# Kernel optimization log

Hardware: AMD Instinct MI355X
Metric: run time of the kernel (lower is better)

Reference implementation:

```python
import jax, jax.numpy as jnp
import numpy as np

# Module hyperparameters (init_kwargs)
NCE_K = 256      # samples per example (col 0 = positive)
NCE_T = 0.07     # temperature
EPS = 1e-7

# Problem sizes
B = 4096         # batch
D = 128          # embedding dim
N = 1_000_000    # memory bank size


def setup_inputs() -> dict:
    key = jax.random.key(0)
    k1, k2, k3, k4 = jax.random.split(key, 4)
    x = jax.random.normal(k1, (B, D), dtype=jnp.float32)
    targets = jax.random.randint(k2, (B,), 0, N)
    memory = jax.random.normal(k3, (N, D), dtype=jnp.float32) * 0.05
    # uniform multinomial-with-replacement sampling == uniform randint
    indices = jax.random.randint(k4, (B, NCE_K), 0, N)
    return {"x": x, "targets": targets, "memory": memory, "indices": indices}


def reference(x, targets, memory, indices):
    # nce_average: overwrite column 0 with the positive index
    idx = indices.at[:, 0].set(targets)              # [B, K]
    weight = memory[idx]                              # [B, K, D] gather
    logits = jnp.einsum('bkd,bd->bk', weight, x) / NCE_T
    sims = jnp.exp(logits)                            # [B, K]
    sims = sims / jnp.sum(sims, axis=1, keepdims=True) * (NCE_K / N)

    # NCE loss: K' = nce_k - 1 noise samples per example
    Kp = NCE_K - 1
    noise = Kp / N
    lnPmt = sims[:, 0] / (sims[:, 0] + noise + EPS)   # [B]
    lnPon = noise / (sims[:, 1:] + noise + EPS)       # [B, K-1]
    loss = -(jnp.log(lnPmt).mean() + jnp.log(lnPon).sum(axis=1).mean())
    return loss
```

## Files before the change

kernel.cpp:

```cpp
#include <hip/hip_runtime.h>

#define B_SZ   4096
#define D_SZ   128
#define K_SZ   256
#define NBUCK  4096
#define BCAP   1024

constexpr float INV_T    = 1.0f / 0.07f;
constexpr float NOISE    = 255.0f / 1000000.0f;
constexpr float EPS_C    = 1e-7f;
constexpr float K_OVER_N = 256.0f / 1000000.0f;


__global__ __launch_bounds__(256) void zero_counters(int* __restrict__ cnt)
{
    const int i = blockIdx.x * 256 + threadIdx.x;
    if (i < NBUCK) cnt[i] = 0;
}

__global__ __launch_bounds__(256, 8) void bin_samples(
    const int* __restrict__ targets,
    const int* __restrict__ indices,
    int*                 __restrict__ cnt,
    unsigned long long*  __restrict__ ent)
{
    const int i = blockIdx.x * 256 + threadIdx.x;
    const int b = i >> 8;
    const int k = i & (K_SZ - 1);
    const int row = (k == 0) ? targets[b] : indices[i];
    const int bu  = row >> 8;
    const int slot = atomicAdd(&cnt[bu], 1);
    if (slot < BCAP)
        ent[(size_t)bu * BCAP + slot] =
            ((unsigned long long)(unsigned)row << 32) | (unsigned)i;
}

__global__ __launch_bounds__(256, 4) void gather_dot(
    const float* __restrict__ x,
    const float* __restrict__ memory,
    const int*                __restrict__ cnt,
    const unsigned long long* __restrict__ ent,
    float*       __restrict__ esims)
{
    const int bu = blockIdx.x;
    const int nb = min(cnt[bu], BCAP);
    if (nb == 0) return;

    const int tid = threadIdx.x;
    const int g   = tid >> 3;
    const int s   = tid & 7;

    for (int base = 0; base < nb; base += 32) {
        const int e  = base + g;
        const int ec = min(e, nb - 1);
        const unsigned long long pk = ent[(size_t)bu * BCAP + ec];
        const int i   = (int)(pk & 0xffffffffu);
        const int row = (int)(pk >> 32);

        const float4* __restrict__ rp =
            (const float4*)(memory + (size_t)row * D_SZ);
        const float4* __restrict__ xp =
            (const float4*)(x + (size_t)(i >> 8) * D_SZ);

        const float4 r0 = rp[0 * 8 + s];
        const float4 r1 = rp[1 * 8 + s];
        const float4 r2 = rp[2 * 8 + s];
        const float4 r3 = rp[3 * 8 + s];
        const float4 x0 = xp[0 * 8 + s];
        const float4 x1 = xp[1 * 8 + s];
        const float4 x2 = xp[2 * 8 + s];
        const float4 x3 = xp[3 * 8 + s];

        float a0 = 0.f, a1 = 0.f;
        a0 = fmaf(r0.x, x0.x, fmaf(r0.y, x0.y, fmaf(r0.z, x0.z, fmaf(r0.w, x0.w, a0))));
        a1 = fmaf(r1.x, x1.x, fmaf(r1.y, x1.y, fmaf(r1.z, x1.z, fmaf(r1.w, x1.w, a1))));
        a0 = fmaf(r2.x, x2.x, fmaf(r2.y, x2.y, fmaf(r2.z, x2.z, fmaf(r2.w, x2.w, a0))));
        a1 = fmaf(r3.x, x3.x, fmaf(r3.y, x3.y, fmaf(r3.z, x3.z, fmaf(r3.w, x3.w, a1))));
        float p = a0 + a1;

        p += __shfl_xor(p, 1, 64);
        p += __shfl_xor(p, 2, 64);
        p += __shfl_xor(p, 4, 64);

        if (s == 0 && e < nb)
            esims[i] = expf(p * INV_T);
    }
}

__global__ __launch_bounds__(256, 8) void reduce_loss(
    const float* __restrict__ esims,
    float*       __restrict__ partial)
{
    __shared__ float s_red[4];
    const int b    = blockIdx.x;
    const int tid  = threadIdx.x;
    const int lane = tid & 63;
    const int wave = tid >> 6;

    const float e = esims[(size_t)b * K_SZ + tid];

    float sum = e;
    #pragma unroll
    for (int m = 32; m >= 1; m >>= 1)
        sum += __shfl_xor(sum, m, 64);
    if (lane == 0) s_red[wave] = sum;
    __syncthreads();
    const float S = s_red[0] + s_red[1] + s_red[2] + s_red[3];

    const float sims = e * (K_OVER_N / S);
    float term = (tid == 0)
        ? logf(sims / (sims + NOISE + EPS_C))
        : logf(NOISE / (sims + NOISE + EPS_C));

    #pragma unroll
    for (int m = 32; m >= 1; m >>= 1)
        term += __shfl_xor(term, m, 64);
    __syncthreads();
    if (lane == 0) s_red[wave] = term;
    __syncthreads();
    if (tid == 0)
        partial[b] = s_red[0] + s_red[1] + s_red[2] + s_red[3];
}

__global__ __launch_bounds__(256) void nce_final(
    const float* __restrict__ partial, float* __restrict__ out)
{
    const int tid = threadIdx.x;
    float s = 0.0f;
    #pragma unroll
    for (int i = tid; i < B_SZ; i += 256)
        s += partial[i];
    #pragma unroll
    for (int m = 32; m >= 1; m >>= 1)
        s += __shfl_xor(s, m, 64);
    __shared__ float sr[4];
    if ((tid & 63) == 0) sr[tid >> 6] = s;
    __syncthreads();
    if (tid == 0)
        out[0] = -(sr[0] + sr[1] + sr[2] + sr[3]) / (float)B_SZ;
}

extern "C" void kernel_launch(void* const* d_in, const int* in_sizes, int n_in,
                              void* d_out, int out_size, void* d_ws, size_t ws_size,
                              hipStream_t stream) {
    const float* x       = (const float*)d_in[0];
    const int*   targets = (const int*)  d_in[1];
    const float* memory  = (const float*)d_in[2];
    const int*   indices = (const int*)  d_in[3];
    float* out = (float*)d_out;

    char* ws = (char*)d_ws;
    int*                cnt     = (int*)ws;
    unsigned long long* ent     = (unsigned long long*)(ws + 16384);
    float*              esims   = (float*)(ws + 16384 + (size_t)NBUCK * BCAP * 8);
    float*              partial = esims + (size_t)B_SZ * K_SZ;

    zero_counters<<<NBUCK / 256, 256, 0, stream>>>(cnt);
    bin_samples<<<(B_SZ * K_SZ) / 256, 256, 0, stream>>>(targets, indices, cnt, ent);
    gather_dot<<<NBUCK, 256, 0, stream>>>(x, memory, cnt, ent, esims);
    reduce_loss<<<B_SZ, 256, 0, stream>>>(esims, partial);
    nce_final<<<1, 256, 0, stream>>>(partial, out);
}
```

Measured before the change: 743.2 us.

## Stage contiguous 64-row memory tiles in LDS instead of random row gathers

Buckets shrink to 64 consecutive memory rows, and each gather_dot block first streams its whole tile into padded shared memory, then computes the dot products from LDS. This turns scattered row gathers into coalesced streaming reads of the full table. It adds about 33KB of LDS per block, which lowers occupancy. It also reads rows that no sample uses, though nearly every bucket is sampled anyway.

```diff
diff --git a/kernel.cpp b/kernel.cpp
--- a/kernel.cpp
+++ b/kernel.cpp
@@ -3,8 +3,13 @@
 #define B_SZ   4096
 #define D_SZ   128
 #define K_SZ   256
-#define NBUCK  4096
-#define BCAP   1024
+#define N_ROWS 1000000
+#define RSHIFT 6
+#define ROWS   (1 << RSHIFT)
+#define NBUCK  16384
+#define NB_USED 15625
+#define BCAP   256
+#define LDS_PITCH 132
 
 constexpr float INV_T    = 1.0f / 0.07f;
 constexpr float NOISE    = 255.0f / 1000000.0f;
@@ -28,7 +33,7 @@
     const int b = i >> 8;
     const int k = i & (K_SZ - 1);
     const int row = (k == 0) ? targets[b] : indices[i];
-    const int bu  = row >> 8;
+    const int bu  = row >> RSHIFT;
     const int slot = atomicAdd(&cnt[bu], 1);
     if (slot < BCAP)
         ent[(size_t)bu * BCAP + slot] =
@@ -42,34 +47,51 @@
     const unsigned long long* __restrict__ ent,
     float*       __restrict__ esims)
 {
+    __shared__ float s_mem[ROWS * LDS_PITCH];
+
     const int bu = blockIdx.x;
     const int nb = min(cnt[bu], BCAP);
+
+    const int row0  = bu << RSHIFT;
+    const int nrows = min(ROWS, N_ROWS - row0);
+    const int tid   = threadIdx.x;
+
+    if (nb > 0) {
+        const float4* __restrict__ src =
+            (const float4*)(memory + (size_t)row0 * D_SZ);
+        const int nchunk = nrows * (D_SZ / 4);
+        for (int idx = tid; idx < nchunk; idx += 256) {
+            const int r = idx >> 5;
+            const int c = idx & 31;
+            const float4 v = src[idx];
+            *(float4*)&s_mem[r * LDS_PITCH + c * 4] = v;
+        }
+    }
+    __syncthreads();
     if (nb == 0) return;
 
-    const int tid = threadIdx.x;
-    const int g   = tid >> 3;
-    const int s   = tid & 7;
+    const int g = tid >> 3;
+    const int s = tid & 7;
 
     for (int base = 0; base < nb; base += 32) {
         const int e  = base + g;
         const int ec = min(e, nb - 1);
         const unsigned long long pk = ent[(size_t)bu * BCAP + ec];
-        const int i   = (int)(pk & 0xffffffffu);
-        const int row = (int)(pk >> 32);
+        const int i    = (int)(pk & 0xffffffffu);
+        const int rloc = ((int)(pk >> 32)) & (ROWS - 1);
 
-        const float4* __restrict__ rp =
-            (const float4*)(memory + (size_t)row * D_SZ);
+        const float* __restrict__ rp = &s_mem[rloc * LDS_PITCH + s * 4];
         const float4* __restrict__ xp =
-            (const float4*)(x + (size_t)(i >> 8) * D_SZ);
+            (const float4*)(x + (size_t)(i >> 8) * D_SZ) + s;
 
-        const float4 r0 = rp[0 * 8 + s];
-        const float4 r1 = rp[1 * 8 + s];
-        const float4 r2 = rp[2 * 8 + s];
-        const float4 r3 = rp[3 * 8 + s];
-        const float4 x0 = xp[0 * 8 + s];
-        const float4 x1 = xp[1 * 8 + s];
-        const float4 x2 = xp[2 * 8 + s];
-        const float4 x3 = xp[3 * 8 + s];
+        const float4 r0 = *(const float4*)(rp + 0);
+        const float4 r1 = *(const float4*)(rp + 32);
+        const float4 r2 = *(const float4*)(rp + 64);
+        const float4 r3 = *(const float4*)(rp + 96);
+        const float4 x0 = xp[0];
+        const float4 x1 = xp[8];
+        const float4 x2 = xp[16];
+        const float4 x3 = xp[24];
 
         float a0 = 0.f, a1 = 0.f;
         a0 = fmaf(r0.x, x0.x, fmaf(r0.y, x0.y, fmaf(r0.z, x0.z, fmaf(r0.w, x0.w, a0))));
@@ -151,13 +173,13 @@
 
     char* ws = (char*)d_ws;
     int*                cnt     = (int*)ws;
-    unsigned long long* ent     = (unsigned long long*)(ws + 16384);
-    float*              esims   = (float*)(ws + 16384 + (size_t)NBUCK * BCAP * 8);
+    unsigned long long* ent     = (unsigned long long*)(ws + 65536);
+    float*              esims   = (float*)(ws + 65536 + (size_t)NBUCK * BCAP * 8);
     float*              partial = esims + (size_t)B_SZ * K_SZ;
 
     zero_counters<<<NBUCK / 256, 256, 0, stream>>>(cnt);
     bin_samples<<<(B_SZ * K_SZ) / 256, 256, 0, stream>>>(targets, indices, cnt, ent);
-    gather_dot<<<NBUCK, 256, 0, stream>>>(x, memory, cnt, ent, esims);
+    gather_dot<<<NB_USED, 256, 0, stream>>>(x, memory, cnt, ent, esims);
     reduce_loss<<<B_SZ, 256, 0, stream>>>(esims, partial);
     nce_final<<<1, 256, 0, stream>>>(partial, out);
 }
```

New measurement: 755.3 us. No clear change (+1.6%).
